# Performance work log

Measured on AMD Instinct MI355X. Metric: run time of the kernel, lower is better.

Reference implementation:

```python
import jax, jax.numpy as jnp
import numpy as np
from jax import lax

ALPHA = -30.0  # softmin temperature from module init
EPS = 1e-4     # matches `+ 0.0001` in _softMinShapeletSeries


def _sliding_softmin(series, shp):
    """Sliding-window mean-squared distance between each shapelet and every
    window of each series, followed by softmin pooling over windows.
    series: [N, T], shp: [K, L] -> [N, K].
    Uses the identity mean((x_win - s)^2) = (sum(x_win^2) - 2<x_win, s> + sum(s^2)) / L
    so the sliding distances become two VALID cross-correlations.
    """
    N, T = series.shape
    K, L = shp.shape
    dn = lax.conv_dimension_numbers((N, 1, T), (K, 1, L), ('NCH', 'OIH', 'NCH'))
    # <x_win, s> for all windows/shapelets: [N, K, W], W = T - L + 1
    xdot = lax.conv_general_dilated(series[:, None, :], shp[:, None, :], (1,), 'VALID',
                                    dimension_numbers=dn)
    dn1 = lax.conv_dimension_numbers((N, 1, T), (1, 1, L), ('NCH', 'OIH', 'NCH'))
    # sum(x_win^2) via correlation with ones kernel: [N, 1, W]
    sumx2 = lax.conv_general_dilated((series * series)[:, None, :],
                                     jnp.ones((1, 1, L), series.dtype), (1,), 'VALID',
                                     dimension_numbers=dn1)
    s2 = jnp.sum(shp * shp, axis=1)  # [K]
    d = (sumx2 - 2.0 * xdot + s2[None, :, None]) / L  # [N, K, W]
    e = jnp.exp(ALPHA * d) + EPS
    return jnp.sum(d * e, axis=2) / jnp.sum(e, axis=2)  # [N, K]


def setup_inputs() -> dict:
    key = jax.random.key(0)
    ks = jax.random.split(key, 6)
    N, T = 512, 2048
    K = 64            # nb_shapelets
    Ls = (32, 64, 96) # shapelet lengths: s * shapelets_size, s = 1..scale
    n_classes = 10
    return {
        'series': jax.random.normal(ks[0], (N, T), jnp.float32),
        'shp1': jax.random.normal(ks[1], (K, Ls[0]), jnp.float32),
        'shp2': jax.random.normal(ks[2], (K, Ls[1]), jnp.float32),
        'shp3': jax.random.normal(ks[3], (K, Ls[2]), jnp.float32),
        'W': jax.random.normal(ks[4], (3 * K, n_classes), jnp.float32) * 0.05,
        'b': jax.random.normal(ks[5], (n_classes,), jnp.float32) * 0.05,
    }


def reference(series, shp1, shp2, shp3, W, b):
    # concat softmin features per scale, in shapelet order (matches torch.cat order)
    sm = jnp.concatenate([_sliding_softmin(series, s) for s in (shp1, shp2, shp3)], axis=1)
    logits = sm @ W + b  # nn.Linear
    return jax.nn.softmax(logits, axis=-1)  # output_size_ > 1 branch
```

## Files before the change

### kernel.cpp

```cpp
#include <hip/hip_runtime.h>
#include <hip/hip_bf16.h>

#define ALPHA_ (-30.0f)
#define EPS_ (1e-4f)
#define LOG2E_ (1.4426950408889634f)

typedef short bf16x8 __attribute__((ext_vector_type(8)));
typedef float f32x4 __attribute__((ext_vector_type(4)));
typedef float f32x2 __attribute__((ext_vector_type(2)));

__device__ __forceinline__ short f2bf(float f) {
  __hip_bfloat16 h = __float2bfloat16(f);
  return __builtin_bit_cast(short, h);
}

__device__ __forceinline__ bf16x8 ld_a(const short* p) {
  int2 lo = *reinterpret_cast<const int2*>(p);
  int2 hi = *reinterpret_cast<const int2*>(p + 4);
  union { int i[4]; bf16x8 v; } u;
  u.i[0] = lo.x; u.i[1] = lo.y; u.i[2] = hi.x; u.i[3] = hi.y;
  return u.v;
}

__device__ __forceinline__ bf16x8 ld_b(const short* p) {
  union { int4 i; bf16x8 v; } u;
  u.i = *reinterpret_cast<const int4*>(p);
  return u.v;
}

#define XC_OFF 0
#define PS_OFF 17536
#define SH_OFF 25744
#define SX_OFF 38032
#define S2_OFF 46224
#define RED_OFF 46480
#define FL_OFF 48528
#define SMEM_BYTES 49296
#define CL 2192

template <int L, int SCALE>
__device__ __forceinline__ void scale_pass(const float* __restrict__ shp,
                                           char* smem, int tid, int lane,
                                           int wv, int col, int kg) {
  constexpr int T = 2048;
  constexpr int W = T - L + 1;
  constexpr int KT = L / 32;
  constexpr int NIT = (W + 63) / 64;
  constexpr int M = W / 64;
  constexpr float CE = ALPHA_ * LOG2E_ / (float)L;
  constexpr float SCL = -2.0f * CE;

  short* xc = (short*)(smem + XC_OFF);
  float* ps = (float*)(smem + PS_OFF);
  short* sh = (short*)(smem + SH_OFF);
  float* sx = (float*)(smem + SX_OFF);
  float* s2 = (float*)(smem + S2_OFF);
  float* red = (float*)(smem + RED_OFF);
  float* fl = (float*)(smem + FL_OFF);

  __syncthreads();
  for (int i = tid; i < 64 * L; i += 256) sh[i] = f2bf(shp[i] * SCL);
  for (int w = tid; w < 2048; w += 256)
    sx[w] = (w < W) ? CE * (ps[w + L] - ps[w]) : 0.f;
  {
    constexpr int LQ = L / 4;
    const float* sp = shp + (tid & 63) * L + wv * LQ;
    float s = 0.f;
#pragma unroll
    for (int l = 0; l < LQ; ++l) s = fmaf(sp[l], sp[l], s);
    red[tid] = s;
  }
  __syncthreads();
  if (tid < 64)
    s2[tid] = CE * (red[tid] + red[tid + 64] + red[tid + 128] + red[tid + 192]);
  __syncthreads();

  bf16x8 bfr[KT][4];
#pragma unroll
  for (int kt = 0; kt < KT; ++kt)
#pragma unroll
    for (int nt = 0; nt < 4; ++nt)
      bfr[kt][nt] = ld_b(sh + (nt * 16 + col) * L + kt * 32 + kg * 8);
  float s2c[4];
#pragma unroll
  for (int nt = 0; nt < 4; ++nt) s2c[nt] = s2[nt * 16 + col];

  const int cc = lane & 3;
  const short* ap = xc + cc * CL + (col - cc) + 8 * kg + wv * 16;
  const float* sp2 = sx + wv * 16 + kg * 4;

  f32x2 esP[4], dsP[4];
#pragma unroll
  for (int nt = 0; nt < 4; ++nt) {
    esP[nt] = (f32x2){0.f, 0.f};
    dsP[nt] = (f32x2){0.f, 0.f};
  }

  int it = 0;
  for (; it < M; ++it) {
    f32x4 acc[4];
#pragma unroll
    for (int nt = 0; nt < 4; ++nt)
      acc[nt] = (f32x4){s2c[nt], s2c[nt], s2c[nt], s2c[nt]};
#pragma unroll
    for (int kt = 0; kt < KT; ++kt) {
      bf16x8 a = ld_a(ap + kt * 32);
#pragma unroll
      for (int nt = 0; nt < 4; ++nt)
        acc[nt] = __builtin_amdgcn_mfma_f32_16x16x32_bf16(a, bfr[kt][nt],
                                                          acc[nt], 0, 0, 0);
    }
    float4 sv = *reinterpret_cast<const float4*>(sp2);
    f32x2 sx01 = {sv.x, sv.y};
    f32x2 sx23 = {sv.z, sv.w};
#pragma unroll
    for (int nt = 0; nt < 4; ++nt) {
      f32x2 u0 = (f32x2){acc[nt][0], acc[nt][1]} + sx01;
      f32x2 u1 = (f32x2){acc[nt][2], acc[nt][3]} + sx23;
      f32x2 e0, e1;
      e0.x = __builtin_amdgcn_exp2f(u0.x);
      e0.y = __builtin_amdgcn_exp2f(u0.y);
      e1.x = __builtin_amdgcn_exp2f(u1.x);
      e1.y = __builtin_amdgcn_exp2f(u1.y);
      e0 += (f32x2){EPS_, EPS_};
      e1 += (f32x2){EPS_, EPS_};
      esP[nt] += e0;
      esP[nt] += e1;
      dsP[nt] = __builtin_elementwise_fma(u0, e0, dsP[nt]);
      dsP[nt] = __builtin_elementwise_fma(u1, e1, dsP[nt]);
    }
    ap += 64;
    sp2 += 64;
  }
  for (; it < NIT; ++it) {
    const int wb = it * 64 + wv * 16 + kg * 4;
    f32x4 acc[4];
#pragma unroll
    for (int nt = 0; nt < 4; ++nt)
      acc[nt] = (f32x4){s2c[nt], s2c[nt], s2c[nt], s2c[nt]};
#pragma unroll
    for (int kt = 0; kt < KT; ++kt) {
      bf16x8 a = ld_a(ap + kt * 32);
#pragma unroll
      for (int nt = 0; nt < 4; ++nt)
        acc[nt] = __builtin_amdgcn_mfma_f32_16x16x32_bf16(a, bfr[kt][nt],
                                                          acc[nt], 0, 0, 0);
    }
    float4 sv = *reinterpret_cast<const float4*>(sp2);
    const float svr[4] = {sv.x, sv.y, sv.z, sv.w};
#pragma unroll
    for (int nt = 0; nt < 4; ++nt) {
#pragma unroll
      for (int r = 0; r < 4; ++r) {
        float u = acc[nt][r] + svr[r];
        float e = __builtin_amdgcn_exp2f(u) + EPS_;
        float em = ((wb + r) < W) ? e : 0.f;
        esP[nt].x += em;
        dsP[nt].x = fmaf(u, em, dsP[nt].x);
      }
    }
    ap += 64;
    sp2 += 64;
  }

  constexpr float ALc = ALPHA_ * LOG2E_;
  float fe[4], fd[4];
#pragma unroll
  for (int nt = 0; nt < 4; ++nt) {
    float es = esP[nt].x + esP[nt].y;
    float ds = dsP[nt].x + dsP[nt].y;
    es += __shfl_xor(es, 16, 64);
    es += __shfl_xor(es, 32, 64);
    ds += __shfl_xor(ds, 16, 64);
    ds += __shfl_xor(ds, 32, 64);
    fe[nt] = es;
    fd[nt] = ds;
  }
  if (lane < 16) {
#pragma unroll
    for (int nt = 0; nt < 4; ++nt) {
      red[wv * 64 + nt * 16 + lane] = fe[nt];
      red[256 + wv * 64 + nt * 16 + lane] = fd[nt];
    }
  }
  __syncthreads();
  if (tid < 64) {
    float es = red[tid] + red[64 + tid] + red[128 + tid] + red[192 + tid];
    float ds = red[256 + tid] + red[320 + tid] + red[384 + tid] + red[448 + tid];
    fl[SCALE * 64 + tid] = ds / (es * ALc);
  }
}

__global__ void __launch_bounds__(256, 2)
feat_kernel(const float* __restrict__ series, const float* __restrict__ shp1,
            const float* __restrict__ shp2, const float* __restrict__ shp3,
            const float* __restrict__ Wm, const float* __restrict__ bvec,
            float* __restrict__ out) {
  __shared__ __align__(16) char smem[SMEM_BYTES];
  constexpr int T = 2048;

  short* xc = (short*)(smem + XC_OFF);
  float* ps = (float*)(smem + PS_OFF);
  float* red = (float*)(smem + RED_OFF);

  const int n = blockIdx.x;
  const int tid = threadIdx.x;
  const int lane = tid & 63;
  const int wv = tid >> 6;
  const int col = lane & 15;
  const int kg = lane >> 4;

  const float* srow = series + (size_t)n * T;
  float4 v0 = *reinterpret_cast<const float4*>(srow + tid * 8);
  float4 v1 = *reinterpret_cast<const float4*>(srow + tid * 8 + 4);
  float xv[8] = {v0.x, v0.y, v0.z, v0.w, v1.x, v1.y, v1.z, v1.w};
  short bv8[12];
#pragma unroll
  for (int i = 0; i < 8; ++i) bv8[i] = f2bf(xv[i]);
  if (tid < 255) {
    float4 ve = *reinterpret_cast<const float4*>(srow + tid * 8 + 8);
    bv8[8] = f2bf(ve.x); bv8[9] = f2bf(ve.y);
    bv8[10] = f2bf(ve.z); bv8[11] = f2bf(ve.w);
  } else {
    bv8[8] = bv8[9] = bv8[10] = bv8[11] = 0;
  }

  float loc[8];
  float run = 0.f;
#pragma unroll
  for (int i = 0; i < 8; ++i) {
    run = fmaf(xv[i], xv[i], run);
    loc[i] = run;
  }
  float sc = run;
#pragma unroll
  for (int off = 1; off < 64; off <<= 1) {
    float t = __shfl_up(sc, off, 64);
    if (lane >= off) sc += t;
  }
  if (lane == 63) red[wv] = sc;
  __syncthreads();
  float wb0 = 0.f;
  for (int w = 0; w < wv; ++w) wb0 += red[w];
  float excl = wb0 + sc - run;
#pragma unroll
  for (int i = 0; i < 8; ++i) ps[tid * 8 + 1 + i] = excl + loc[i];
  if (tid == 0) ps[0] = 0.f;

#pragma unroll
  for (int c = 0; c < 4; ++c) {
    union { short s[8]; int4 q; } u;
#pragma unroll
    for (int i = 0; i < 8; ++i) u.s[i] = bv8[i + c];
    *reinterpret_cast<int4*>(xc + c * CL + tid * 8) = u.q;
  }
  if (tid < CL - 2048) {
    int j = 2048 + tid;
#pragma unroll
    for (int c = 0; c < 4; ++c) xc[c * CL + j] = 0;
  }

  scale_pass<32, 0>(shp1, smem, tid, lane, wv, col, kg);
  scale_pass<64, 1>(shp2, smem, tid, lane, wv, col, kg);
  scale_pass<96, 2>(shp3, smem, tid, lane, wv, col, kg);

  __syncthreads();
  float* wl = (float*)(smem + SH_OFF);
  const float* flp = (const float*)(smem + FL_OFF);
  for (int i = tid; i < 1920; i += 256) wl[i] = Wm[i];
  __syncthreads();
  float acc = 0.f;
  if (tid < 10) {
    acc = bvec[tid];
#pragma unroll 8
    for (int j = 0; j < 192; ++j) acc = fmaf(flp[j], wl[j * 10 + tid], acc);
    red[tid] = acc;
  }
  __syncthreads();
  if (tid < 10) {
    float m = red[0];
#pragma unroll
    for (int j = 1; j < 10; ++j) m = fmaxf(m, red[j]);
    float s = 0.f;
#pragma unroll
    for (int j = 0; j < 10; ++j)
      s += __builtin_amdgcn_exp2f((red[j] - m) * LOG2E_);
    out[(size_t)n * 10 + tid] = __builtin_amdgcn_exp2f((acc - m) * LOG2E_) / s;
  }
}

extern "C" void kernel_launch(void* const* d_in, const int* in_sizes, int n_in,
                              void* d_out, int out_size, void* d_ws, size_t ws_size,
                              hipStream_t stream) {
  const float* series = (const float*)d_in[0];
  const float* shp1 = (const float*)d_in[1];
  const float* shp2 = (const float*)d_in[2];
  const float* shp3 = (const float*)d_in[3];
  const float* Wm = (const float*)d_in[4];
  const float* bv = (const float*)d_in[5];
  float* out = (float*)d_out;

  feat_kernel<<<512, 256, 0, stream>>>(series, shp1, shp2, shp3, Wm, bv, out);
}
```

Before: 53.57 us.

## Split scales across a 2D grid and move logits/softmax into a separate kernel

The fused per-series kernel, which processed all three shapelet scales sequentially, is split into a grid of 512x3 blocks, one per series and scale. Each block writes its 64 softmin features to a workspace buffer, and a second small kernel computes the linear layer and softmax per series. Shared memory is reduced by aliasing the shapelet and window-sum buffers, with launch bounds raised to 3 blocks per CU. This adds parallelism and occupancy, but each block now reloads the series and recomputes the prefix sums and bf16 shifted copies three times. It also adds a second kernel launch and a global round trip for the features.

Result: slower. 57.98 us (+8.2%).

```diff
diff --git a/kernel.cpp b/kernel.cpp
--- a/kernel.cpp
+++ b/kernel.cpp
@@ -30,18 +30,16 @@
 
 #define XC_OFF 0
 #define PS_OFF 17536
-#define SH_OFF 25744
-#define SX_OFF 38032
-#define S2_OFF 46224
-#define RED_OFF 46480
-#define FL_OFF 48528
-#define SMEM_BYTES 49296
+#define R2_OFF 25744
+#define S2_OFF 38032
+#define RED_OFF 38288
+#define SMEM_BYTES 40352
 #define CL 2192
 
 template <int L, int SCALE>
-__device__ __forceinline__ void scale_pass(const float* __restrict__ shp,
-                                           char* smem, int tid, int lane,
-                                           int wv, int col, int kg) {
+__device__ __forceinline__ void feat_impl(const float* __restrict__ series,
+                                          const float* __restrict__ shp,
+                                          float* __restrict__ F, char* smem) {
   constexpr int T = 2048;
   constexpr int W = T - L + 1;
   constexpr int KT = L / 32;
@@ -52,27 +50,90 @@
 
   short* xc = (short*)(smem + XC_OFF);
   float* ps = (float*)(smem + PS_OFF);
-  short* sh = (short*)(smem + SH_OFF);
-  float* sx = (float*)(smem + SX_OFF);
+  short* sh = (short*)(smem + R2_OFF);
+  float* sx = (float*)(smem + R2_OFF);
   float* s2 = (float*)(smem + S2_OFF);
   float* red = (float*)(smem + RED_OFF);
-  float* fl = (float*)(smem + FL_OFF);
-
-  __syncthreads();
-  for (int i = tid; i < 64 * L; i += 256) sh[i] = f2bf(shp[i] * SCL);
-  for (int w = tid; w < 2048; w += 256)
-    sx[w] = (w < W) ? CE * (ps[w + L] - ps[w]) : 0.f;
+
+  const int n = blockIdx.x;
+  const int tid = threadIdx.x;
+  const int lane = tid & 63;
+  const int wv = tid >> 6;
+  const int col = lane & 15;
+  const int kg = lane >> 4;
+
+  const float* srow = series + (size_t)n * T;
+  float4 v0 = *reinterpret_cast<const float4*>(srow + tid * 8);
+  float4 v1 = *reinterpret_cast<const float4*>(srow + tid * 8 + 4);
+  float xv[8] = {v0.x, v0.y, v0.z, v0.w, v1.x, v1.y, v1.z, v1.w};
+  short bv8[12];
+#pragma unroll
+  for (int i = 0; i < 8; ++i) bv8[i] = f2bf(xv[i]);
+  if (tid < 255) {
+    float4 ve = *reinterpret_cast<const float4*>(srow + tid * 8 + 8);
+    bv8[8] = f2bf(ve.x); bv8[9] = f2bf(ve.y);
+    bv8[10] = f2bf(ve.z); bv8[11] = f2bf(ve.w);
+  } else {
+    bv8[8] = bv8[9] = bv8[10] = bv8[11] = 0;
+  }
+
+  float loc[8];
+  float run = 0.f;
+#pragma unroll
+  for (int i = 0; i < 8; ++i) {
+    run = fmaf(xv[i], xv[i], run);
+    loc[i] = run;
+  }
+  float sc = run;
+#pragma unroll
+  for (int off = 1; off < 64; off <<= 1) {
+    float t = __shfl_up(sc, off, 64);
+    if (lane >= off) sc += t;
+  }
+  if (lane == 63) red[wv] = sc;
+  __syncthreads();
+  float wb0 = 0.f;
+  for (int w = 0; w < wv; ++w) wb0 += red[w];
+  float excl = wb0 + sc - run;
+#pragma unroll
+  for (int i = 0; i < 8; ++i) ps[tid * 8 + 1 + i] = excl + loc[i];
+  if (tid == 0) ps[0] = 0.f;
+
+#pragma unroll
+  for (int c = 0; c < 4; ++c) {
+    union { short s[8]; int4 q; } u;
+#pragma unroll
+    for (int i = 0; i < 8; ++i) u.s[i] = bv8[i + c];
+    *reinterpret_cast<int4*>(xc + c * CL + tid * 8) = u.q;
+  }
+  if (tid < CL - 2048) {
+    int j = 2048 + tid;
+#pragma unroll
+    for (int c = 0; c < 4; ++c) xc[c * CL + j] = 0;
+  }
+
+  {
+    constexpr int NE = 64 * L;
+    for (int i4 = tid * 4; i4 < NE; i4 += 1024) {
+      float4 v = *reinterpret_cast<const float4*>(shp + i4);
+      union { short s[4]; int2 q; } u;
+      u.s[0] = f2bf(v.x * SCL); u.s[1] = f2bf(v.y * SCL);
+      u.s[2] = f2bf(v.z * SCL); u.s[3] = f2bf(v.w * SCL);
+      *reinterpret_cast<int2*>(sh + i4) = u.q;
+    }
+  }
   {
     constexpr int LQ = L / 4;
-    const float* sp = shp + (tid & 63) * L + wv * LQ;
+    const float* sp = shp + lane * L + wv * LQ;
     float s = 0.f;
 #pragma unroll
     for (int l = 0; l < LQ; ++l) s = fmaf(sp[l], sp[l], s);
-    red[tid] = s;
+    red[256 + tid] = s;
   }
   __syncthreads();
   if (tid < 64)
-    s2[tid] = CE * (red[tid] + red[tid + 64] + red[tid + 128] + red[tid + 192]);
+    s2[tid] = CE * (red[256 + tid] + red[320 + tid] + red[384 + tid] +
+                    red[448 + tid]);
   __syncthreads();
 
   bf16x8 bfr[KT][4];
@@ -84,6 +145,11 @@
   float s2c[4];
 #pragma unroll
   for (int nt = 0; nt < 4; ++nt) s2c[nt] = s2[nt * 16 + col];
+  __syncthreads();
+
+  for (int w = tid; w < 2048; w += 256)
+    sx[w] = (w < W) ? CE * (ps[w + L] - ps[w]) : 0.f;
+  __syncthreads();
 
   const int cc = lane & 3;
   const short* ap = xc + cc * CL + (col - cc) + 8 * kg + wv * 16;
@@ -176,6 +242,7 @@
     fe[nt] = es;
     fd[nt] = ds;
   }
+  __syncthreads();
   if (lane < 16) {
 #pragma unroll
     for (int nt = 0; nt < 4; ++nt) {
@@ -187,106 +254,59 @@
   if (tid < 64) {
     float es = red[tid] + red[64 + tid] + red[128 + tid] + red[192 + tid];
     float ds = red[256 + tid] + red[320 + tid] + red[384 + tid] + red[448 + tid];
-    fl[SCALE * 64 + tid] = ds / (es * ALc);
-  }
-}
-
-__global__ void __launch_bounds__(256, 2)
+    F[n * 192 + SCALE * 64 + tid] = ds / (es * ALc);
+  }
+}
+
+__global__ void __launch_bounds__(256, 3)
 feat_kernel(const float* __restrict__ series, const float* __restrict__ shp1,
             const float* __restrict__ shp2, const float* __restrict__ shp3,
-            const float* __restrict__ Wm, const float* __restrict__ bvec,
-            float* __restrict__ out) {
+            float* __restrict__ F) {
   __shared__ __align__(16) char smem[SMEM_BYTES];
-  constexpr int T = 2048;
-
-  short* xc = (short*)(smem + XC_OFF);
-  float* ps = (float*)(smem + PS_OFF);
-  float* red = (float*)(smem + RED_OFF);
-
-  const int n = blockIdx.x;
+  if (blockIdx.y == 0)
+    feat_impl<32, 0>(series, shp1, F, smem);
+  else if (blockIdx.y == 1)
+    feat_impl<64, 1>(series, shp2, F, smem);
+  else
+    feat_impl<96, 2>(series, shp3, F, smem);
+}
+
+__global__ void __launch_bounds__(256) logits_kernel(const float* __restrict__ F,
+                                                     const float* __restrict__ Wm,
+                                                     const float* __restrict__ bv,
+                                                     float* __restrict__ out) {
+  __shared__ float Ws[1920];
+  __shared__ float bs[16];
   const int tid = threadIdx.x;
-  const int lane = tid & 63;
-  const int wv = tid >> 6;
-  const int col = lane & 15;
-  const int kg = lane >> 4;
-
-  const float* srow = series + (size_t)n * T;
-  float4 v0 = *reinterpret_cast<const float4*>(srow + tid * 8);
-  float4 v1 = *reinterpret_cast<const float4*>(srow + tid * 8 + 4);
-  float xv[8] = {v0.x, v0.y, v0.z, v0.w, v1.x, v1.y, v1.z, v1.w};
-  short bv8[12];
-#pragma unroll
-  for (int i = 0; i < 8; ++i) bv8[i] = f2bf(xv[i]);
-  if (tid < 255) {
-    float4 ve = *reinterpret_cast<const float4*>(srow + tid * 8 + 8);
-    bv8[8] = f2bf(ve.x); bv8[9] = f2bf(ve.y);
-    bv8[10] = f2bf(ve.z); bv8[11] = f2bf(ve.w);
-  } else {
-    bv8[8] = bv8[9] = bv8[10] = bv8[11] = 0;
-  }
-
-  float loc[8];
-  float run = 0.f;
-#pragma unroll
-  for (int i = 0; i < 8; ++i) {
-    run = fmaf(xv[i], xv[i], run);
-    loc[i] = run;
-  }
-  float sc = run;
-#pragma unroll
-  for (int off = 1; off < 64; off <<= 1) {
-    float t = __shfl_up(sc, off, 64);
-    if (lane >= off) sc += t;
-  }
-  if (lane == 63) red[wv] = sc;
-  __syncthreads();
-  float wb0 = 0.f;
-  for (int w = 0; w < wv; ++w) wb0 += red[w];
-  float excl = wb0 + sc - run;
-#pragma unroll
-  for (int i = 0; i < 8; ++i) ps[tid * 8 + 1 + i] = excl + loc[i];
-  if (tid == 0) ps[0] = 0.f;
-
-#pragma unroll
-  for (int c = 0; c < 4; ++c) {
-    union { short s[8]; int4 q; } u;
-#pragma unroll
-    for (int i = 0; i < 8; ++i) u.s[i] = bv8[i + c];
-    *reinterpret_cast<int4*>(xc + c * CL + tid * 8) = u.q;
-  }
-  if (tid < CL - 2048) {
-    int j = 2048 + tid;
-#pragma unroll
-    for (int c = 0; c < 4; ++c) xc[c * CL + j] = 0;
-  }
-
-  scale_pass<32, 0>(shp1, smem, tid, lane, wv, col, kg);
-  scale_pass<64, 1>(shp2, smem, tid, lane, wv, col, kg);
-  scale_pass<96, 2>(shp3, smem, tid, lane, wv, col, kg);
-
-  __syncthreads();
-  float* wl = (float*)(smem + SH_OFF);
-  const float* flp = (const float*)(smem + FL_OFF);
-  for (int i = tid; i < 1920; i += 256) wl[i] = Wm[i];
-  __syncthreads();
-  float acc = 0.f;
-  if (tid < 10) {
-    acc = bvec[tid];
-#pragma unroll 8
-    for (int j = 0; j < 192; ++j) acc = fmaf(flp[j], wl[j * 10 + tid], acc);
-    red[tid] = acc;
-  }
-  __syncthreads();
-  if (tid < 10) {
-    float m = red[0];
-#pragma unroll
-    for (int j = 1; j < 10; ++j) m = fmaxf(m, red[j]);
-    float s = 0.f;
-#pragma unroll
-    for (int j = 0; j < 10; ++j)
-      s += __builtin_amdgcn_exp2f((red[j] - m) * LOG2E_);
-    out[(size_t)n * 10 + tid] = __builtin_amdgcn_exp2f((acc - m) * LOG2E_) / s;
-  }
+  for (int i = tid; i < 1920; i += 256) Ws[i] = Wm[i];
+  if (tid < 10) bs[tid] = bv[tid];
+  __syncthreads();
+
+  const int n = blockIdx.x * 256 + tid;
+  float acc[10];
+#pragma unroll
+  for (int c = 0; c < 10; ++c) acc[c] = bs[c];
+  const float* f = F + n * 192;
+  for (int j = 0; j < 192; j += 4) {
+    float4 v = *reinterpret_cast<const float4*>(f + j);
+#pragma unroll
+    for (int c = 0; c < 10; ++c)
+      acc[c] += v.x * Ws[(j + 0) * 10 + c] + v.y * Ws[(j + 1) * 10 + c] +
+                v.z * Ws[(j + 2) * 10 + c] + v.w * Ws[(j + 3) * 10 + c];
+  }
+  float m = acc[0];
+#pragma unroll
+  for (int c = 1; c < 10; ++c) m = fmaxf(m, acc[c]);
+  float s = 0.f;
+  float e[10];
+#pragma unroll
+  for (int c = 0; c < 10; ++c) {
+    e[c] = exp2f((acc[c] - m) * LOG2E_);
+    s += e[c];
+  }
+  float inv = 1.f / s;
+#pragma unroll
+  for (int c = 0; c < 10; ++c) out[n * 10 + c] = e[c] * inv;
 }
 
 extern "C" void kernel_launch(void* const* d_in, const int* in_sizes, int n_in,
@@ -299,6 +319,8 @@
   const float* Wm = (const float*)d_in[4];
   const float* bv = (const float*)d_in[5];
   float* out = (float*)d_out;
-
-  feat_kernel<<<512, 256, 0, stream>>>(series, shp1, shp2, shp3, Wm, bv, out);
-}
+  float* F = (float*)d_ws;
+
+  feat_kernel<<<dim3(512, 3), 256, 0, stream>>>(series, shp1, shp2, shp3, F);
+  logits_kernel<<<2, 256, 0, stream>>>(F, Wm, bv, out);
+}
```
